# Optimization experiments

Measured on AMD Instinct MI355X. Metric: run time of the kernel, lower is better.

## Reference

```python
import jax, jax.numpy as jnp
import numpy as np
from jax.scipy.stats import norm

N_NODES = 8192   # n_nodes; also fs (receivers = arange(fs) indexes Z)
E = 262144       # n_entries: timestamped interaction events in the batch
BS = 4096        # len(nodes)
N_SEND = 2048    # unique senders used in integral term
K = 8            # n_change_points passed to __init__ -> K+1 change points
TMAX = 100.0
PENALTY = 10.0


def setup_inputs() -> dict:
    key = jax.random.key(0)
    ks = jax.random.split(key, 8)
    Z = jax.random.normal(ks[0], (N_NODES, 2, K + 1), jnp.float32)
    beta = jax.random.normal(ks[1], (), jnp.float32)
    timestamps = jax.random.uniform(ks[2], (E,), jnp.float32, 0.0, TMAX)
    senders = jax.random.randint(ks[3], (E,), 0, N_NODES, jnp.int32)
    receivers = jax.random.randint(ks[4], (E,), 0, N_NODES, jnp.int32)
    nodes = jax.random.randint(ks[5], (BS,), 0, N_NODES, jnp.int32)
    senders_unique = jnp.sort(jax.random.permutation(ks[6], N_NODES)[:N_SEND]).astype(jnp.int32)
    change_points = (jnp.arange(K + 1, dtype=jnp.float32) / K) * (TMAX + 1e-4)
    return dict(Z=Z, beta=beta, timestamps=timestamps, senders=senders,
                receivers=receivers, nodes=nodes, senders_unique=senders_unique,
                change_points=change_points, fs=N_NODES)


def _rowdot(a, b):  # [n,2],[n,2] -> [n]
    return jnp.sum(a * b, axis=1)


def _negloglike(Z, beta, timestamps, change_points, senders, receivers, nodes,
                senders_unique, fs):
    seg = change_points[1] - change_points[0]
    # gaussian random-walk prior on trajectories of the batch nodes
    prior = PENALTY * (jnp.sum(Z[nodes, :, 0] ** 2)
                       + jnp.sum((Z[nodes, :, 1:] - Z[nodes, :, :-1]) ** 2))
    # time-bin gather + linear interpolation per event
    kappa = jnp.floor(timestamps / seg).astype(jnp.int32)
    d = timestamps / seg - kappa  # deltas in [0,1)
    od = 1.0 - d
    Zs_c = Z[senders, :, kappa]      # [E,2]
    Zs_n = Z[senders, :, kappa + 1]
    Zr_c = Z[receivers, :, kappa]
    Zr_n = Z[receivers, :, kappa + 1]
    flt = (od ** 2 * (2 * _rowdot(Zs_c, Zr_c) - _rowdot(Zs_c, Zs_c) - _rowdot(Zr_c, Zr_c))
           + 2 * d * od * (_rowdot(Zs_c, Zr_n) + _rowdot(Zs_n, Zr_c)
                           - _rowdot(Zs_c, Zs_n) - _rowdot(Zr_c, Zr_n))
           + d ** 2 * (2 * _rowdot(Zs_n, Zr_n) - _rowdot(Zs_n, Zs_n) - _rowdot(Zr_n, Zr_n)))
    # integral term: scan over change points (keeps one [S,fs] tile set live)
    Zu = jnp.moveaxis(Z[senders_unique], 2, 0)  # [K+1, S, 2]
    Zr = jnp.moveaxis(Z[:fs], 2, 0)             # [K+1, fs, 2]
    dts = change_points[1:] - change_points[:-1]
    xs = (Zu[:-1], Zu[1:], Zr[:-1], Zr[1:], dts)

    def step(acc, x):
        Zs0, Zs1, Zr0, Zr1, dt = x
        D = (_rowdot(Zs0, Zs0)[:, None] + _rowdot(Zr0, Zr0)[None, :]
             - 2 * Zs0 @ Zr0.T)
        DZs = Zs1 - Zs0
        DZr = Zr1 - Zr0
        S = (_rowdot(DZs, DZs)[:, None] + _rowdot(DZr, DZr)[None, :]
             - 2 * DZs @ DZr.T)
        C = (DZs @ Zr0.T + Zs0 @ DZr.T
             - _rowdot(DZs, Zs0)[:, None] - _rowdot(DZr, Zr0)[None, :])
        mask = (D > 0.0) & (S > 0.0)  # replaces boolean filtering in torch
        Ss = jnp.where(mask, S, 1.0)  # safe denominator; masked out below
        mu = C / Ss
        sigma = jnp.sqrt(0.5 / Ss)
        val = (jnp.exp(Ss * mu ** 2 - D) * sigma
               * (norm.cdf((1.0 - mu) / sigma) - norm.cdf(-mu / sigma)) * dt)
        return acc + 0.5 * jnp.sum(jnp.where(mask, val, 0.0)), None

    integral, _ = jax.lax.scan(step, jnp.float32(0.0), xs)
    n_entries = jnp.float32(timestamps.shape[0])
    sqrt_2pi = jnp.sqrt(jnp.float32(2.0 * np.pi))
    scale = fs / nodes.shape[0]  # fs / bs
    return scale * (prior - beta * n_entries - jnp.sum(flt)
                    + sqrt_2pi * jnp.exp(beta) * integral)


def reference(Z, beta, timestamps, senders, receivers, nodes, senders_unique,
              change_points, fs):
    return _negloglike(Z, beta, timestamps, change_points, senders, receivers,
                       nodes, senders_unique, fs)
```

## Files before the change

kernel.cpp:

```cpp
#include <hip/hip_runtime.h>

#define EDGES   262144
#define CTPB    256
#define SCHUNK  256
#define NINT    2048
#define NFLT    (EDGES / CTPB)
#define NPRI    16
#define NBLK    (NINT + NFLT + NPRI)

typedef float v2f __attribute__((ext_vector_type(2)));

__device__ __forceinline__ float fast_rsq(float x) { return __builtin_amdgcn_rsqf(x); }

__device__ __forceinline__ v2f erf_poly2(v2f x) {
    v2f c;
    c.x = __builtin_amdgcn_fmed3f(x.x, -2.0f, 2.0f);
    c.y = __builtin_amdgcn_fmed3f(x.y, -2.0f, 2.0f);
    v2f t = c * c;
    v2f p = t * 0.0011996f - 0.0165450f;
    p = p * t + 0.100174f;
    p = p * t - 0.370237f;
    p = p * t + 1.127915f;
    return c * p;
}

template <int NW>
__device__ __forceinline__ float block_reduce(float v, float* sm) {
    #pragma unroll
    for (int o = 32; o > 0; o >>= 1) v += __shfl_down(v, o, 64);
    int lane = threadIdx.x & 63;
    int wid  = threadIdx.x >> 6;
    if (lane == 0) sm[wid] = v;
    __syncthreads();
    float r = 0.0f;
    if (threadIdx.x == 0) {
        #pragma unroll
        for (int w = 0; w < NW; ++w) r += sm[w];
    }
    return r;
}

__global__ __launch_bounds__(CTPB) void k_mega(const float* __restrict__ Z,
        const float* __restrict__ ts, const int* __restrict__ snd,
        const int* __restrict__ rcv, const int* __restrict__ nodes,
        const int* __restrict__ su, const float* __restrict__ cp,
        float* __restrict__ part, int mode) {
    __shared__ __align__(16) float sZx[SCHUNK];
    __shared__ __align__(16) float sZy[SCHUNK];
    __shared__ __align__(16) float sDx[SCHUNK];
    __shared__ __align__(16) float sDy[SCHUNK];
    __shared__ float smr[CTPB / 64];
    const int bid = blockIdx.x;
    const int tid = threadIdx.x;
    float r;
    int slot;

    if (bid < NINT) {
        const int k  = bid >> 8;
        const int sc = (bid >> 5) & 7;
        const int rb = bid & 31;
        {
            int n = su[sc * SCHUNK + tid];
            const float* z = Z + n * 18 + k;
            float zx = z[0], zy = z[9];
            sZx[tid] = zx; sZy[tid] = zy;
            sDx[tid] = z[1] - zx; sDy[tid] = z[10] - zy;
        }
        const float* zr = Z + (rb * CTPB + tid) * 18 + k;
        float rzx = zr[0], rzy = zr[9];
        float rdx = zr[1] - rzx, rdy = zr[10] - rzy;
        __syncthreads();

        const v2f* pZx = (const v2f*)sZx;
        const v2f* pZy = (const v2f*)sZy;
        const v2f* pDx = (const v2f*)sDx;
        const v2f* pDy = (const v2f*)sDy;
        float s0 = 0.0f, s1 = 0.0f;
        #pragma unroll 4
        for (int i = 0; i < SCHUNK / 2; ++i) {
            v2f wx = pZx[i] - rzx;
            v2f wy = pZy[i] - rzy;
            v2f vx = pDx[i] - rdx;
            v2f vy = pDy[i] - rdy;
            v2f D  = wx * wx + wy * wy;
            v2f S  = vx * vx + vy * vy;
            v2f mc = vx * wx + vy * wy;
            v2f rsq;
            rsq.x = fast_rsq(S.x);
            rsq.y = fast_rsq(S.y);
            v2f u  = -mc * rsq;
            v2f rt = S * rsq;
            v2f ea = u * u - D;
            v2f ex;
            ex.x = __expf(ea.x);
            ex.y = __expf(ea.y);
            v2f e = erf_poly2(rt - u) + erf_poly2(u);
            v2f q = ex * rsq * e;
            s0 += (D.x > 0.0f && S.x > 0.0f) ? q.x : 0.0f;
            s1 += (D.y > 0.0f && S.y > 0.0f) ? q.y : 0.0f;
        }
        r = block_reduce<CTPB / 64>(s0 + s1, smr);
        slot = 2;
    } else if (bid < NINT + NFLT) {
        int e = (bid - NINT) * CTPB + tid;
        float seg = cp[1] - cp[0];
        float x   = ts[e] / seg;
        float kf  = floorf(x);
        int kappa = (int)kf;
        float d   = x - kf;
        float od  = 1.0f - d;
        int sb = snd[e] * 18, rbse = rcv[e] * 18;
        float ux = Z[sb + kappa]     - Z[rbse + kappa];
        float uy = Z[sb + 9 + kappa] - Z[rbse + 9 + kappa];
        float vx = Z[sb + kappa + 1]     - Z[rbse + kappa + 1];
        float vy = Z[sb + 9 + kappa + 1] - Z[rbse + 9 + kappa + 1];
        float wx = od * ux + d * vx;
        float wy = od * uy + d * vy;
        r = block_reduce<CTPB / 64>(-fmaf(wx, wx, wy * wy), smr);
        slot = 1;
    } else {
        int i = (bid - NINT - NFLT) * CTPB + tid;
        int n = nodes[i];
        const float* z = Z + n * 18;
        float s = 0.0f;
        #pragma unroll
        for (int d = 0; d < 2; ++d) {
            float prev = z[d * 9];
            s = fmaf(prev, prev, s);
            #pragma unroll
            for (int k = 1; k <= 8; ++k) {
                float cur = z[d * 9 + k];
                float df  = cur - prev;
                s = fmaf(df, df, s);
                prev = cur;
            }
        }
        r = block_reduce<CTPB / 64>(s, smr);
        slot = 0;
    }
    if (tid == 0) {
        if (mode) part[bid] = r;
        else      atomicAdd(part + slot, r);
    }
}

__global__ __launch_bounds__(CTPB) void k_final(const float* __restrict__ ws,
        int mode, const float* __restrict__ betap, const int* __restrict__ fsp,
        const float* __restrict__ cp, float* __restrict__ out,
        float n_entries, float bs) {
    __shared__ float sm0[CTPB / 64], sm1[CTPB / 64], sm2[CTPB / 64];
    int tid = threadIdx.x;
    float pr, fl, qq;
    if (mode) {
        float q = 0.0f, f = 0.0f, p = 0.0f;
        for (int i = tid; i < NBLK; i += CTPB) {
            float v = ws[i];
            if (i < NINT)             q += v;
            else if (i < NINT + NFLT) f += v;
            else                      p += v;
        }
        qq = block_reduce<CTPB / 64>(q, sm0);
        fl = block_reduce<CTPB / 64>(f, sm1);
        pr = block_reduce<CTPB / 64>(p, sm2);
    } else {
        pr = ws[0]; fl = ws[1]; qq = ws[2];
    }
    if (tid == 0) {
        float prior  = 10.0f * pr;
        float beta   = betap[0];
        float fs     = (float)fsp[0];
        float seg    = cp[1] - cp[0];
        float integral = 0.17677669529663687f * seg * qq;
        const float sqrt2pi = 2.5066282746310002f;
        float res = prior - beta * n_entries - fl + sqrt2pi * expf(beta) * integral;
        out[0] = (fs / bs) * res;
    }
}

extern "C" void kernel_launch(void* const* d_in, const int* in_sizes, int n_in,
                              void* d_out, int out_size, void* d_ws, size_t ws_size,
                              hipStream_t stream) {
    const float* Z    = (const float*)d_in[0];
    const float* beta = (const float*)d_in[1];
    const float* ts   = (const float*)d_in[2];
    const int*   snd  = (const int*)d_in[3];
    const int*   rcv  = (const int*)d_in[4];
    const int*   nodes= (const int*)d_in[5];
    const int*   su   = (const int*)d_in[6];
    const float* cp   = (const float*)d_in[7];
    const int*   fs   = (const int*)d_in[8];
    float* acc = (float*)d_ws;

    const int mode = (ws_size >= NBLK * sizeof(float)) ? 1 : 0;
    if (!mode) hipMemsetAsync(acc, 0, 3 * sizeof(float), stream);
    k_mega<<<NBLK, CTPB, 0, stream>>>(Z, ts, snd, rcv, nodes, su, cp, acc, mode);
    k_final<<<1, CTPB, 0, stream>>>(acc, mode, beta, fs, cp, (float*)d_out,
                                    (float)in_sizes[2], (float)in_sizes[5]);
}
```

Before: 164.2 us.

## Fold exp scaling into Z and drop per-pair mask via self-term correction

Pre-scales the Z and delta values by 1/sqrt(ln2), so the exponent can go straight to the hardware exp2 and the erf polynomial is refit to the scaled argument. The per-pair mask for D>0 and S>0 is replaced by clamping S to a tiny floor. The known self-pair contributions (2048 senders × 8 segments) are then subtracted analytically in the final kernel in double precision. The inner loop also switches from packed v2f math to scalar FMAs over float4 LDS loads with four accumulators. This saves the exp multiply and the compare/select work per pair. The risk is that the correction only cancels exactly when the sole zero-distance pairs are self pairs, and that the large self terms may cause cancellation error.

```diff
diff --git a/kernel.cpp b/kernel.cpp
--- a/kernel.cpp
+++ b/kernel.cpp
@@ -8,20 +8,40 @@
 #define NPRI    16
 #define NBLK    (NINT + NFLT + NPRI)
 
-typedef float v2f __attribute__((ext_vector_type(2)));
+#define KS      1.2011224087864498f
+#define SCLAMP  0x1p-60f
 
 __device__ __forceinline__ float fast_rsq(float x) { return __builtin_amdgcn_rsqf(x); }
-
-__device__ __forceinline__ v2f erf_poly2(v2f x) {
-    v2f c;
-    c.x = __builtin_amdgcn_fmed3f(x.x, -2.0f, 2.0f);
-    c.y = __builtin_amdgcn_fmed3f(x.y, -2.0f, 2.0f);
-    v2f t = c * c;
-    v2f p = t * 0.0011996f - 0.0165450f;
-    p = p * t + 0.100174f;
-    p = p * t - 0.370237f;
-    p = p * t + 1.127915f;
+__device__ __forceinline__ float fast_ex2(float x) { return __builtin_amdgcn_exp2f(x); }
+
+__device__ __forceinline__ float erf_s(float x) {
+    const float C0 =  0.93905091f;
+    const float C1 = -0.21365741f;
+    const float C2 =  0.04006996f;
+    const float C3 = -0.00458728f;
+    const float C4 =  0.00023054f;
+    const float CL =  2.4022448f;
+    float c = __builtin_amdgcn_fmed3f(x, -CL, CL);
+    float t = c * c;
+    float p = fmaf(t, fmaf(t, fmaf(t, fmaf(t, C4, C3), C2), C1), C0);
     return c * p;
+}
+
+__device__ __forceinline__ float pair_term(float szx, float szy, float sdx, float sdy,
+                                           float rzx, float rzy, float rdx, float rdy,
+                                           float acc) {
+    float wx = szx - rzx, wy = szy - rzy;
+    float vx = sdx - rdx, vy = sdy - rdy;
+    float D  = fmaf(wy, wy, wx * wx);
+    float S  = fmaf(vy, vy, vx * vx);
+    float mc = fmaf(vy, wy, vx * wx);
+    float Sc = fmaxf(S, SCLAMP);
+    float rsq = fast_rsq(Sc);
+    float g  = mc * rsq;
+    float rt = Sc * rsq;
+    float ex = fast_ex2(fmaf(g, g, -D));
+    float e  = erf_s(rt + g) - erf_s(g);
+    return fmaf(ex * rsq, e, acc);
 }
 
 template <int NW>
@@ -45,10 +65,10 @@
         const int* __restrict__ rcv, const int* __restrict__ nodes,
         const int* __restrict__ su, const float* __restrict__ cp,
         float* __restrict__ part, int mode) {
-    __shared__ __align__(16) float sZx[SCHUNK];
-    __shared__ __align__(16) float sZy[SCHUNK];
-    __shared__ __align__(16) float sDx[SCHUNK];
-    __shared__ __align__(16) float sDy[SCHUNK];
+    __shared__ float4 sZx4[SCHUNK / 4];
+    __shared__ float4 sZy4[SCHUNK / 4];
+    __shared__ float4 sDx4[SCHUNK / 4];
+    __shared__ float4 sDy4[SCHUNK / 4];
     __shared__ float smr[CTPB / 64];
     const int bid = blockIdx.x;
     const int tid = threadIdx.x;
@@ -62,44 +82,31 @@
         {
             int n = su[sc * SCHUNK + tid];
             const float* z = Z + n * 18 + k;
-            float zx = z[0], zy = z[9];
-            sZx[tid] = zx; sZy[tid] = zy;
-            sDx[tid] = z[1] - zx; sDy[tid] = z[10] - zy;
+            float zx = z[0] * KS, zy = z[9] * KS;
+            ((float*)sZx4)[tid] = zx;
+            ((float*)sZy4)[tid] = zy;
+            ((float*)sDx4)[tid] = fmaf(z[1],  KS, -zx);
+            ((float*)sDy4)[tid] = fmaf(z[10], KS, -zy);
         }
         const float* zr = Z + (rb * CTPB + tid) * 18 + k;
-        float rzx = zr[0], rzy = zr[9];
-        float rdx = zr[1] - rzx, rdy = zr[10] - rzy;
+        float rzx = zr[0] * KS, rzy = zr[9] * KS;
+        float rdx = fmaf(zr[1],  KS, -rzx);
+        float rdy = fmaf(zr[10], KS, -rzy);
         __syncthreads();
 
-        const v2f* pZx = (const v2f*)sZx;
-        const v2f* pZy = (const v2f*)sZy;
-        const v2f* pDx = (const v2f*)sDx;
-        const v2f* pDy = (const v2f*)sDy;
-        float s0 = 0.0f, s1 = 0.0f;
-        #pragma unroll 4
-        for (int i = 0; i < SCHUNK / 2; ++i) {
-            v2f wx = pZx[i] - rzx;
-            v2f wy = pZy[i] - rzy;
-            v2f vx = pDx[i] - rdx;
-            v2f vy = pDy[i] - rdy;
-            v2f D  = wx * wx + wy * wy;
-            v2f S  = vx * vx + vy * vy;
-            v2f mc = vx * wx + vy * wy;
-            v2f rsq;
-            rsq.x = fast_rsq(S.x);
-            rsq.y = fast_rsq(S.y);
-            v2f u  = -mc * rsq;
-            v2f rt = S * rsq;
-            v2f ea = u * u - D;
-            v2f ex;
-            ex.x = __expf(ea.x);
-            ex.y = __expf(ea.y);
-            v2f e = erf_poly2(rt - u) + erf_poly2(u);
-            v2f q = ex * rsq * e;
-            s0 += (D.x > 0.0f && S.x > 0.0f) ? q.x : 0.0f;
-            s1 += (D.y > 0.0f && S.y > 0.0f) ? q.y : 0.0f;
-        }
-        r = block_reduce<CTPB / 64>(s0 + s1, smr);
+        float s0 = 0.0f, s1 = 0.0f, s2 = 0.0f, s3 = 0.0f;
+        #pragma unroll 2
+        for (int i = 0; i < SCHUNK / 4; ++i) {
+            float4 azx = sZx4[i];
+            float4 azy = sZy4[i];
+            float4 adx = sDx4[i];
+            float4 ady = sDy4[i];
+            s0 = pair_term(azx.x, azy.x, adx.x, ady.x, rzx, rzy, rdx, rdy, s0);
+            s1 = pair_term(azx.y, azy.y, adx.y, ady.y, rzx, rzy, rdx, rdy, s1);
+            s2 = pair_term(azx.z, azy.z, adx.z, ady.z, rzx, rzy, rdx, rdy, s2);
+            s3 = pair_term(azx.w, azy.w, adx.w, ady.w, rzx, rzy, rdx, rdy, s3);
+        }
+        r = block_reduce<CTPB / 64>((s0 + s1) + (s2 + s3), smr);
         slot = 2;
     } else if (bid < NINT + NFLT) {
         int e = (bid - NINT) * CTPB + tid;
@@ -166,11 +173,18 @@
         pr = ws[0]; fl = ws[1]; qq = ws[2];
     }
     if (tid == 0) {
+        float rsqs = fast_rsq(SCLAMP);
+        float rts  = SCLAMP * rsqs;
+        float es   = erf_s(rts);
+        double qself = (double)rsqs * (double)es;
+        double Q = (double)qq - 16384.0 * qself;
+
         float prior  = 10.0f * pr;
         float beta   = betap[0];
         float fs     = (float)fsp[0];
         float seg    = cp[1] - cp[0];
-        float integral = 0.17677669529663687f * seg * qq;
+        const double CQ = 0.17677669529663687 * 1.2011224087864498;
+        float integral = (float)(CQ * (double)seg * Q);
         const float sqrt2pi = 2.5066282746310002f;
         float res = prior - beta * n_entries - fl + sqrt2pi * expf(beta) * integral;
         out[0] = (fs / bs) * res;
```

Result: slower. 171.0 us (+4.1%).

## Register-tile two receivers per thread and fuse final reduction via last-block atomic

Applied to the files above, without the earlier changes.

Each integral block now handles 512 receivers (two per thread) against the shared sender chunk, halving the integral block count and reusing each shared-memory sender load for two pair evaluations. The separate finalize kernel is removed: blocks atomically accumulate into three slots, and the last block, detected with a ticket counter, computes the output. The vectorised float2 math becomes scalar fmaf-based code. This trades a kernel launch and per-block partial writes for a memset plus atomics, and float atomic accumulation order becomes nondeterministic.

```diff
diff --git a/kernel.cpp b/kernel.cpp
--- a/kernel.cpp
+++ b/kernel.cpp
@@ -3,7 +3,8 @@
 #define EDGES   262144
 #define CTPB    256
 #define SCHUNK  256
-#define NINT    2048
+#define RTILE   512
+#define NINT    1024
 #define NFLT    (EDGES / CTPB)
 #define NPRI    16
 #define NBLK    (NINT + NFLT + NPRI)
@@ -12,16 +13,30 @@
 
 __device__ __forceinline__ float fast_rsq(float x) { return __builtin_amdgcn_rsqf(x); }
 
-__device__ __forceinline__ v2f erf_poly2(v2f x) {
-    v2f c;
-    c.x = __builtin_amdgcn_fmed3f(x.x, -2.0f, 2.0f);
-    c.y = __builtin_amdgcn_fmed3f(x.y, -2.0f, 2.0f);
-    v2f t = c * c;
-    v2f p = t * 0.0011996f - 0.0165450f;
-    p = p * t + 0.100174f;
-    p = p * t - 0.370237f;
-    p = p * t + 1.127915f;
+__device__ __forceinline__ float erf_poly(float x) {
+    float c = __builtin_amdgcn_fmed3f(x, -2.0f, 2.0f);
+    float t = c * c;
+    float p = fmaf(t, fmaf(t, fmaf(t, fmaf(t, 0.0011996f, -0.0165450f),
+                                   0.100174f), -0.370237f), 1.127915f);
     return c * p;
+}
+
+__device__ __forceinline__ float pterm(float szx, float szy, float sdx, float sdy,
+                                       float rzx, float rzy, float rdx, float rdy,
+                                       float acc) {
+    float wx = szx - rzx, wy = szy - rzy;
+    float vx = sdx - rdx, vy = sdy - rdy;
+    float D  = fmaf(wy, wy, wx * wx);
+    float S  = fmaf(vy, vy, vx * vx);
+    float mc = fmaf(vy, wy, vx * wx);
+    float rsq = fast_rsq(S);
+    float u  = -mc * rsq;
+    float rt = S * rsq;
+    float ex = __expf(fmaf(u, u, -D));
+    float e  = erf_poly(rt - u) + erf_poly(u);
+    float q  = ex * rsq * e;
+    float qm = (fminf(D, S) > 0.0f) ? q : 0.0f;
+    return acc + qm;
 }
 
 template <int NW>
@@ -40,25 +55,29 @@
     return r;
 }
 
-__global__ __launch_bounds__(CTPB) void k_mega(const float* __restrict__ Z,
+__global__ __launch_bounds__(CTPB) void k_all(const float* __restrict__ Z,
         const float* __restrict__ ts, const int* __restrict__ snd,
         const int* __restrict__ rcv, const int* __restrict__ nodes,
         const int* __restrict__ su, const float* __restrict__ cp,
-        float* __restrict__ part, int mode) {
+        const float* __restrict__ betap, const int* __restrict__ fsp,
+        unsigned* __restrict__ ws, float* __restrict__ out,
+        float n_entries, float bs) {
     __shared__ __align__(16) float sZx[SCHUNK];
     __shared__ __align__(16) float sZy[SCHUNK];
     __shared__ __align__(16) float sDx[SCHUNK];
     __shared__ __align__(16) float sDy[SCHUNK];
     __shared__ float smr[CTPB / 64];
+    __shared__ int isLast;
+    float* acc = (float*)(ws + 4);
     const int bid = blockIdx.x;
     const int tid = threadIdx.x;
     float r;
     int slot;
 
     if (bid < NINT) {
-        const int k  = bid >> 8;
-        const int sc = (bid >> 5) & 7;
-        const int rb = bid & 31;
+        const int k  = bid >> 7;
+        const int sc = (bid >> 4) & 7;
+        const int rb = bid & 15;
         {
             int n = su[sc * SCHUNK + tid];
             const float* z = Z + n * 18 + k;
@@ -66,40 +85,31 @@
             sZx[tid] = zx; sZy[tid] = zy;
             sDx[tid] = z[1] - zx; sDy[tid] = z[10] - zy;
         }
-        const float* zr = Z + (rb * CTPB + tid) * 18 + k;
-        float rzx = zr[0], rzy = zr[9];
-        float rdx = zr[1] - rzx, rdy = zr[10] - rzy;
+        const float* zr0 = Z + (rb * RTILE + tid) * 18 + k;
+        const float* zr1 = zr0 + 256 * 18;
+        float r0zx = zr0[0], r0zy = zr0[9];
+        float r0dx = zr0[1] - r0zx, r0dy = zr0[10] - r0zy;
+        float r1zx = zr1[0], r1zy = zr1[9];
+        float r1dx = zr1[1] - r1zx, r1dy = zr1[10] - r1zy;
         __syncthreads();
 
         const v2f* pZx = (const v2f*)sZx;
         const v2f* pZy = (const v2f*)sZy;
         const v2f* pDx = (const v2f*)sDx;
         const v2f* pDy = (const v2f*)sDy;
-        float s0 = 0.0f, s1 = 0.0f;
-        #pragma unroll 4
+        float a00 = 0.0f, a01 = 0.0f, a10 = 0.0f, a11 = 0.0f;
+        #pragma unroll 2
         for (int i = 0; i < SCHUNK / 2; ++i) {
-            v2f wx = pZx[i] - rzx;
-            v2f wy = pZy[i] - rzy;
-            v2f vx = pDx[i] - rdx;
-            v2f vy = pDy[i] - rdy;
-            v2f D  = wx * wx + wy * wy;
-            v2f S  = vx * vx + vy * vy;
-            v2f mc = vx * wx + vy * wy;
-            v2f rsq;
-            rsq.x = fast_rsq(S.x);
-            rsq.y = fast_rsq(S.y);
-            v2f u  = -mc * rsq;
-            v2f rt = S * rsq;
-            v2f ea = u * u - D;
-            v2f ex;
-            ex.x = __expf(ea.x);
-            ex.y = __expf(ea.y);
-            v2f e = erf_poly2(rt - u) + erf_poly2(u);
-            v2f q = ex * rsq * e;
-            s0 += (D.x > 0.0f && S.x > 0.0f) ? q.x : 0.0f;
-            s1 += (D.y > 0.0f && S.y > 0.0f) ? q.y : 0.0f;
+            v2f azx = pZx[i];
+            v2f azy = pZy[i];
+            v2f adx = pDx[i];
+            v2f ady = pDy[i];
+            a00 = pterm(azx.x, azy.x, adx.x, ady.x, r0zx, r0zy, r0dx, r0dy, a00);
+            a01 = pterm(azx.y, azy.y, adx.y, ady.y, r0zx, r0zy, r0dx, r0dy, a01);
+            a10 = pterm(azx.x, azy.x, adx.x, ady.x, r1zx, r1zy, r1dx, r1dy, a10);
+            a11 = pterm(azx.y, azy.y, adx.y, ady.y, r1zx, r1zy, r1dx, r1dy, a11);
         }
-        r = block_reduce<CTPB / 64>(s0 + s1, smr);
+        r = block_reduce<CTPB / 64>((a00 + a01) + (a10 + a11), smr);
         slot = 2;
     } else if (bid < NINT + NFLT) {
         int e = (bid - NINT) * CTPB + tid;
@@ -138,38 +148,21 @@
         r = block_reduce<CTPB / 64>(s, smr);
         slot = 0;
     }
+
     if (tid == 0) {
-        if (mode) part[bid] = r;
-        else      atomicAdd(part + slot, r);
+        atomicAdd(acc + slot, r);
+        __threadfence();
+        unsigned old = atomicAdd(ws, 1u);
+        isLast = (old == NBLK - 1);
     }
-}
-
-__global__ __launch_bounds__(CTPB) void k_final(const float* __restrict__ ws,
-        int mode, const float* __restrict__ betap, const int* __restrict__ fsp,
-        const float* __restrict__ cp, float* __restrict__ out,
-        float n_entries, float bs) {
-    __shared__ float sm0[CTPB / 64], sm1[CTPB / 64], sm2[CTPB / 64];
-    int tid = threadIdx.x;
-    float pr, fl, qq;
-    if (mode) {
-        float q = 0.0f, f = 0.0f, p = 0.0f;
-        for (int i = tid; i < NBLK; i += CTPB) {
-            float v = ws[i];
-            if (i < NINT)             q += v;
-            else if (i < NINT + NFLT) f += v;
-            else                      p += v;
-        }
-        qq = block_reduce<CTPB / 64>(q, sm0);
-        fl = block_reduce<CTPB / 64>(f, sm1);
-        pr = block_reduce<CTPB / 64>(p, sm2);
-    } else {
-        pr = ws[0]; fl = ws[1]; qq = ws[2];
-    }
-    if (tid == 0) {
-        float prior  = 10.0f * pr;
-        float beta   = betap[0];
-        float fs     = (float)fsp[0];
-        float seg    = cp[1] - cp[0];
+    __syncthreads();
+    if (isLast && tid == 0) {
+        __threadfence();
+        float pr = acc[0], fl = acc[1], qq = acc[2];
+        float prior = 10.0f * pr;
+        float beta  = betap[0];
+        float fs    = (float)fsp[0];
+        float seg   = cp[1] - cp[0];
         float integral = 0.17677669529663687f * seg * qq;
         const float sqrt2pi = 2.5066282746310002f;
         float res = prior - beta * n_entries - fl + sqrt2pi * expf(beta) * integral;
@@ -189,11 +182,9 @@
     const int*   su   = (const int*)d_in[6];
     const float* cp   = (const float*)d_in[7];
     const int*   fs   = (const int*)d_in[8];
-    float* acc = (float*)d_ws;
 
-    const int mode = (ws_size >= NBLK * sizeof(float)) ? 1 : 0;
-    if (!mode) hipMemsetAsync(acc, 0, 3 * sizeof(float), stream);
-    k_mega<<<NBLK, CTPB, 0, stream>>>(Z, ts, snd, rcv, nodes, su, cp, acc, mode);
-    k_final<<<1, CTPB, 0, stream>>>(acc, mode, beta, fs, cp, (float*)d_out,
-                                    (float)in_sizes[2], (float)in_sizes[5]);
+    (void)hipMemsetAsync(d_ws, 0, 32, stream);
+    k_all<<<NBLK, CTPB, 0, stream>>>(Z, ts, snd, rcv, nodes, su, cp, beta, fs,
+                                     (unsigned*)d_ws, (float*)d_out,
+                                     (float)in_sizes[2], (float)in_sizes[5]);
 }
```

Measured after the change: 191.2 us. +16.4%, slower.
